# Kernel optimization log

Hardware: AMD Instinct MI355X
Metric: run time of the kernel (lower is better)

The kernel has to match this reference:

```python
import jax, jax.numpy as jnp
import numpy as np

VOXEL = 0.1          # superpoint_voxel_size
NUM_BATCHES = 4      # B (batch indices in coords[:,0] are in [0, B))


def setup_inputs() -> dict:
    key = jax.random.key(0)
    k1, k2, k3, k4, k5, k6, k7 = jax.random.split(key, 7)
    N, D = 1_000_000, 64
    batch_ids = jax.random.randint(k1, (N,), 0, NUM_BATCHES).astype(jnp.float32)
    xyz = jax.random.uniform(k2, (N, 3), dtype=jnp.float32) * 50.0  # 50m scene
    coords = jnp.concatenate([batch_ids[:, None], xyz], axis=1)      # (N,4)
    features = jax.random.normal(k3, (N, D), dtype=jnp.float32)
    s1 = 1.0 / np.sqrt(3.0)
    s2 = 1.0 / np.sqrt(D)
    W1 = jax.random.uniform(k4, (3, D), minval=-s1, maxval=s1, dtype=jnp.float32)
    b1 = jax.random.uniform(k5, (D,), minval=-s1, maxval=s1, dtype=jnp.float32)
    W2 = jax.random.uniform(k6, (D, D), minval=-s2, maxval=s2, dtype=jnp.float32)
    b2 = jax.random.uniform(k7, (D,), minval=-s2, maxval=s2, dtype=jnp.float32)
    return {"coords": coords, "features": features, "W1": W1, "b1": b1, "W2": W2, "b2": b2}


def reference(coords, features, W1, b1, W2, b2):
    N, D = features.shape
    batch_ids = coords[:, 0].astype(jnp.int32)          # (N,)
    xyz = coords[:, 1:4]                                 # (N,3)
    q = jnp.floor(xyz / VOXEL).astype(jnp.int32)         # voxel quantization
    combined = jnp.concatenate([batch_ids[:, None], q], axis=1)  # (N,4) int32 keys

    # torch.unique(dim=0, return_inverse=True): lexicographically sorted unique
    # rows. We pad to a fixed S=N segments (fill rows sorted to the tail via a
    # max sentinel); `valid` masks out the padding.
    SENT = jnp.iinfo(jnp.int32).max
    unique_sp, sp_to_point = jnp.unique(
        combined, axis=0, size=N, fill_value=SENT, return_inverse=True)
    sp_to_point = sp_to_point.reshape(-1)                # (N,)

    counts = jax.ops.segment_sum(jnp.ones((N,), jnp.float32), sp_to_point, num_segments=N)
    valid = counts > 0
    c = jnp.maximum(counts, 1.0)[:, None]                # clamp(min=1)

    sp_features = jax.ops.segment_sum(features, sp_to_point, num_segments=N) / c  # (N,D) mean
    sp_centers = jax.ops.segment_sum(xyz, sp_to_point, num_segments=N) / c        # (N,3) mean

    # pos_enc: Linear(3,D) -> ReLU -> Linear(D,D)
    pos = jnp.maximum(sp_centers @ W1 + b1, 0.0) @ W2 + b2
    sp_features = jnp.where(valid[:, None], sp_features + pos, 0.0)
    sp_centers = jnp.where(valid[:, None], sp_centers, 0.0)

    # batch_offsets: cumulative superpoint counts per batch (padding -> dump bin B)
    sp_batch = jnp.where(valid, unique_sp[:, 0], NUM_BATCHES)
    per_batch = jax.ops.segment_sum(jnp.ones((N,), jnp.int32), sp_batch,
                                    num_segments=NUM_BATCHES + 1)[:NUM_BATCHES]
    batch_offsets = jnp.concatenate([jnp.zeros((1,), jnp.int32), jnp.cumsum(per_batch)])
    return sp_features, sp_centers, sp_to_point, batch_offsets
```

## Files before the change

### kernel.cpp

```cpp
#include <hip/hip_runtime.h>
#include <stdint.h>


static constexpr uint32_t NWORDS = 1u << 24;
static constexpr uint32_t NBLK   = NWORDS / 1024;
static constexpr uint32_t MCAP   = 65536;

typedef __attribute__((ext_vector_type(8))) short short8;
typedef __attribute__((ext_vector_type(4))) float f32x4;

__device__ __forceinline__ short f2bf(float x) {
    union { float f; uint32_t u; } v; v.f = x;
    uint32_t u = v.u;
    uint32_t r = (u + 0x7FFFu + ((u >> 16) & 1u)) >> 16;
    return (short)r;
}

__device__ __forceinline__ uint32_t point_key(float4 c) {
    uint32_t b  = (uint32_t)(int)c.x;
    uint32_t qx = (uint32_t)(int)floorf(c.y / 0.1f);
    uint32_t qy = (uint32_t)(int)floorf(c.z / 0.1f);
    uint32_t qz = (uint32_t)(int)floorf(c.w / 0.1f);
    return (b << 27) | (qx << 18) | (qy << 9) | qz;
}

__global__ void k0_w2t(const float* __restrict__ W2, short* __restrict__ W2T) {
    int t = blockIdx.x * 256 + threadIdx.x;
    if (t < 4096) {
        int col = t >> 6, k = t & 63;
        W2T[col * 64 + k] = f2bf(W2[k * 64 + col]);
    }
}

__global__ void k1_keys(const float4* __restrict__ coords, uint32_t* __restrict__ bitmap, int N) {
    int i = blockIdx.x * blockDim.x + threadIdx.x;
    if (i >= N) return;
    uint32_t key = point_key(coords[i]);
    atomicOr(&bitmap[key >> 5], 1u << (key & 31u));
}

__global__ __launch_bounds__(256) void k2a_blockscan(
        const uint4* __restrict__ bm4, uint16_t* __restrict__ scan4,
        uint32_t* __restrict__ bsum) {
    int t = threadIdx.x;
    int lane = t & 63, wid = t >> 6;
    uint4 v = bm4[(size_t)blockIdx.x * 256 + t];
    uint32_t pc = __popc(v.x) + __popc(v.y) + __popc(v.z) + __popc(v.w);
    uint32_t sc = pc;
    #pragma unroll
    for (int off = 1; off < 64; off <<= 1) {
        uint32_t n = __shfl_up(sc, off);
        if (lane >= off) sc += n;
    }
    __shared__ uint32_t wt[4];
    if (lane == 63) wt[wid] = sc;
    __syncthreads();
    uint32_t wbase = 0;
    #pragma unroll
    for (int w = 0; w < 4; ++w) wbase += (w < wid) ? wt[w] : 0u;
    scan4[(size_t)blockIdx.x * 256 + t] = (uint16_t)(wbase + sc - pc);
    if (t == 255) bsum[blockIdx.x] = wbase + sc;
}

__global__ void k2b_topscan(const uint32_t* __restrict__ bsum, uint32_t* __restrict__ bscan) {
    __shared__ uint32_t s[1024];
    int t = threadIdx.x;
    uint32_t base = (uint32_t)t * 16u;
    const uint4* b4 = (const uint4*)(bsum + base);
    uint32_t sum = 0;
    #pragma unroll
    for (int k = 0; k < 4; ++k) { uint4 v = b4[k]; sum += v.x + v.y + v.z + v.w; }
    s[t] = sum;
    __syncthreads();
    for (int off = 1; off < 1024; off <<= 1) {
        uint32_t v = (t >= off) ? s[t - off] : 0u;
        __syncthreads();
        s[t] += v;
        __syncthreads();
    }
    uint32_t run = s[t] - sum;
    for (int k = 0; k < 16; ++k) { bscan[base + k] = run; run += bsum[base + k]; }
    if (t == 1023) bscan[16384] = run;
}

__global__ void k3a_rank(const float4* __restrict__ coords,
                         uint32_t* __restrict__ ranks,
                         const uint32_t* __restrict__ bitmap,
                         const uint16_t* __restrict__ scan4,
                         const uint32_t* __restrict__ bscan,
                         float* __restrict__ sums,
                         uint32_t* __restrict__ inv,
                         uint32_t* __restrict__ slotmap,
                         uint32_t* __restrict__ mctr,
                         float* __restrict__ msum,
                         float* __restrict__ mfeat,
                         float* __restrict__ out_sp, int N) {
    int i = blockIdx.x * blockDim.x + threadIdx.x;
    if (i >= N) return;
    float4 c = coords[i];
    uint32_t key = point_key(c);
    uint32_t w = key >> 5, bit = key & 31u;
    uint4 q = *(const uint4*)(bitmap + (w & ~3u));
    uint32_t wd[4] = {q.x, q.y, q.z, q.w};
    uint32_t idx = w & 3u;
    uint32_t r = bscan[w >> 10] + (uint32_t)scan4[w >> 2];
    uint32_t cur = 0;
    #pragma unroll
    for (uint32_t j = 0; j < 4; ++j) {
        r += (j < idx) ? __popc(wd[j]) : 0u;
        cur = (j == idx) ? wd[j] : cur;
    }
    r += __popc(cur & ((1u << bit) - 1u));
    ranks[i] = r;
    inv[r] = (uint32_t)i;
    out_sp[i] = (float)r;
    float* s4 = sums + 4u * (size_t)r;
    float old = atomicAdd(s4 + 0, 1.0f);
    s4[1] = c.y; s4[2] = c.z; s4[3] = c.w;
    if (old == 1.0f) {
        uint32_t slot = atomicAdd(mctr, 1u);
        if (slot < MCAP) {
            slotmap[r] = slot + 1u;
            float4 z = make_float4(0.f, 0.f, 0.f, 0.f);
            *(float4*)(msum + 4u * (size_t)slot) = z;
            float4* fz = (float4*)(mfeat + 64u * (size_t)slot);
            #pragma unroll
            for (int qq = 0; qq < 16; ++qq) fz[qq] = z;
        }
    }
}

__global__ void k3fix(const float4* __restrict__ coords,
                      const float* __restrict__ features,
                      const uint32_t* __restrict__ ranks,
                      const uint32_t* __restrict__ slotmap,
                      const float4* __restrict__ sums,
                      float* __restrict__ msum,
                      float* __restrict__ mfeat, int N) {
    int i = blockIdx.x * blockDim.x + threadIdx.x;
    if (i >= N) return;
    uint32_t r = ranks[i];
    uint32_t sl = slotmap[r];
    if (sl == 0) return;
    sl -= 1u;
    float cnt = sums[r].x;
    float4 c = coords[i];
    float* m = msum + 4u * (size_t)sl;
    atomicAdd(m + 0, c.y);
    atomicAdd(m + 1, c.z);
    atomicAdd(m + 2, c.w);
    float iv = 1.0f / cnt;
    const float* frow = features + (size_t)i * 64;
    float* orow = mfeat + (size_t)sl * 64;
    #pragma unroll 1
    for (int qq = 0; qq < 64; ++qq) atomicAdd(&orow[qq], frow[qq] * iv);
}

__global__ __launch_bounds__(256) void k5_fused(
        const f32x4* __restrict__ features4,
        const uint32_t* __restrict__ inv,
        const float4* __restrict__ sums,
        const uint32_t* __restrict__ slotmap,
        const float4* __restrict__ msum,
        const f32x4* __restrict__ mfeat4,
        const float* __restrict__ W1, const float* __restrict__ b1,
        const short* __restrict__ W2T, const float* __restrict__ b2,
        f32x4* __restrict__ out_feat4, float* __restrict__ out_cent, int N) {
    int lane = threadIdx.x & 63;
    int rows_base = blockIdx.x * 256 + (threadIdx.x >> 6) * 64;

    float4 sg4[4]; float cntg[4]; uint32_t invg[4];
    #pragma unroll
    for (int g = 0; g < 4; ++g) {
        int rg = rows_base + (g << 4) + (lane & 15);
        int rgc = rg < N ? rg : N - 1;
        sg4[g] = sums[rgc];
        cntg[g] = sg4[g].x;
        invg[g] = inv[rgc];
    }

    float scx[4], scy[4], scz[4];
    #pragma unroll
    for (int g = 0; g < 4; ++g) {
        int rg = rows_base + (g << 4) + (lane & 15);
        int rgc = rg < N ? rg : N - 1;
        float sx = sg4[g].y, sy = sg4[g].z, sz = sg4[g].w;
        if (cntg[g] > 1.5f) {
            float4 m = msum[slotmap[rgc] - 1u];
            sx = m.x; sy = m.y; sz = m.z;
        }
        float ic = cntg[g] > 0.f ? 1.f / cntg[g] : 0.f;
        scx[g] = sx * ic; scy[g] = sy * ic; scz[g] = sz * ic;
    }

    int my = rows_base + lane;
    if (my < N) {
        float4 s4 = sums[my];
        float sx = s4.y, sy = s4.z, sz = s4.w;
        if (s4.x > 1.5f) {
            float4 m = msum[slotmap[my] - 1u];
            sx = m.x; sy = m.y; sz = m.z;
        }
        float ic = s4.x > 0.f ? 1.f / s4.x : 0.f;
        out_cent[3 * (size_t)my + 0] = sx * ic;
        out_cent[3 * (size_t)my + 1] = sy * ic;
        out_cent[3 * (size_t)my + 2] = sz * ic;
    }

    f32x4 acc[4][4];
    #pragma unroll
    for (int cg = 0; cg < 4; ++cg) {
        f32x4 bv = ((const f32x4*)b2)[(cg << 2) + (lane >> 4)];
        #pragma unroll
        for (int g = 0; g < 4; ++g)
            acc[g][cg] = bv;
    }

    #pragma unroll
    for (int s = 0; s < 2; ++s) {
        int kb = s * 32 + ((lane >> 4) << 3);
        float4 tx0 = *(const float4*)(W1 + kb),       tx1 = *(const float4*)(W1 + kb + 4);
        float4 ty0 = *(const float4*)(W1 + 64 + kb),  ty1 = *(const float4*)(W1 + 64 + kb + 4);
        float4 tz0 = *(const float4*)(W1 + 128 + kb), tz1 = *(const float4*)(W1 + 128 + kb + 4);
        float4 tb0 = *(const float4*)(b1 + kb),       tb1 = *(const float4*)(b1 + kb + 4);
        float w1x[8] = {tx0.x, tx0.y, tx0.z, tx0.w, tx1.x, tx1.y, tx1.z, tx1.w};
        float w1y[8] = {ty0.x, ty0.y, ty0.z, ty0.w, ty1.x, ty1.y, ty1.z, ty1.w};
        float w1z[8] = {tz0.x, tz0.y, tz0.z, tz0.w, tz1.x, tz1.y, tz1.z, tz1.w};
        float b1v[8] = {tb0.x, tb0.y, tb0.z, tb0.w, tb1.x, tb1.y, tb1.z, tb1.w};

        short8 afrag[4];
        #pragma unroll
        for (int cg = 0; cg < 4; ++cg) {
            int col = (cg << 4) | (lane & 15);
            afrag[cg] = *(const short8*)(W2T + col * 64 + kb);
        }

        #pragma unroll
        for (int g = 0; g < 4; ++g) {
            short8 hf;
            #pragma unroll
            for (int j = 0; j < 8; ++j) {
                float h = fmaf(scz[g], w1z[j], fmaf(scy[g], w1y[j], fmaf(scx[g], w1x[j], b1v[j])));
                hf[j] = f2bf(fmaxf(h, 0.0f));
            }
            #pragma unroll
            for (int cg = 0; cg < 4; ++cg)
                acc[g][cg] = __builtin_amdgcn_mfma_f32_16x16x32_bf16(afrag[cg], hf, acc[g][cg], 0, 0, 0);
        }
    }

    #pragma unroll
    for (int g = 0; g < 4; ++g) {
        int gr = rows_base + (g << 4) + (lane & 15);
        if (gr >= N) continue;
        float cnt = cntg[g];
        f32x4 v[4];
        #pragma unroll
        for (int cg = 0; cg < 4; ++cg) v[cg] = acc[g][cg];
        if (cnt == 0.0f) {
            #pragma unroll
            for (int cg = 0; cg < 4; ++cg) v[cg] = (f32x4){0.f, 0.f, 0.f, 0.f};
        } else if (cnt == 1.0f) {
            size_t fb = (size_t)invg[g] * 16 + (lane >> 4);
            #pragma unroll
            for (int cg = 0; cg < 4; ++cg) v[cg] += features4[fb + (cg << 2)];
        } else {
            size_t mb = (size_t)(slotmap[gr] - 1u) * 16 + (lane >> 4);
            #pragma unroll
            for (int cg = 0; cg < 4; ++cg) v[cg] += mfeat4[mb + (cg << 2)];
        }
        size_t ob = (size_t)gr * 16 + (lane >> 4);
        #pragma unroll
        for (int cg = 0; cg < 4; ++cg)
            __builtin_nontemporal_store(v[cg], out_feat4 + ob + (cg << 2));
    }
}

__global__ void k6_offsets(const uint32_t* __restrict__ bscan, float* __restrict__ out_off) {
    int t = threadIdx.x;
    if (t < 5) {
        uint32_t v;
        if (t == 0)      v = 0u;
        else if (t == 4) v = bscan[16384];
        else             v = bscan[(uint32_t)t << 12];
        out_off[t] = (float)v;
    }
}

extern "C" void kernel_launch(void* const* d_in, const int* in_sizes, int n_in,
                              void* d_out, int out_size, void* d_ws, size_t ws_size,
                              hipStream_t stream) {
    const float4* coords = (const float4*)d_in[0];
    const float*  feats  = (const float*)d_in[1];
    const float*  W1 = (const float*)d_in[2];
    const float*  b1 = (const float*)d_in[3];
    const float*  W2 = (const float*)d_in[4];
    const float*  b2 = (const float*)d_in[5];
    int N = in_sizes[0] / 4;

    char* ws = (char*)d_ws;
    size_t o = 0;
    uint32_t* bitmap = (uint32_t*)(ws + o); o += (size_t)NWORDS * 4;
    uint16_t* scan4  = (uint16_t*)(ws + o); o += (size_t)(NWORDS / 4) * 2;
    uint32_t* bsum   = (uint32_t*)(ws + o); o += (size_t)NBLK * 4;
    uint32_t* bscan  = (uint32_t*)(ws + o); o += (size_t)(NBLK + 1) * 4;
    o = (o + 15) & ~(size_t)15;
    uint32_t* ranks  = (uint32_t*)(ws + o); o += (size_t)N * 4;
    o = (o + 15) & ~(size_t)15;
    float*    sums   = (float*)(ws + o);    o += (size_t)N * 16;
    uint32_t* inv    = (uint32_t*)(ws + o); o += (size_t)N * 4;
    o = (o + 15) & ~(size_t)15;
    short*    W2T    = (short*)(ws + o);    o += 8192;
    size_t multi_base = o;
    uint32_t* slotmap = (uint32_t*)(ws + o); o += (size_t)N * 4;
    uint32_t* mctr    = (uint32_t*)(ws + o); o += 16;
    size_t multi_size = o - multi_base;
    float*    msum    = (float*)(ws + o);    o += (size_t)MCAP * 16;
    float*    mfeat   = (float*)(ws + o);    o += (size_t)MCAP * 256;

    float* out_feat = (float*)d_out;
    float* out_cent = out_feat + (size_t)N * 64;
    float* out_sp   = out_cent + (size_t)N * 3;
    float* out_off  = out_sp + N;

    hipMemsetAsync(bitmap, 0, (size_t)NWORDS * 4, stream);
    hipMemsetAsync(sums, 0, (size_t)N * 16, stream);
    hipMemsetAsync(ws + multi_base, 0, multi_size, stream);

    int nb = (N + 255) / 256;
    k0_w2t<<<16, 256, 0, stream>>>(W2, W2T);
    k1_keys<<<nb, 256, 0, stream>>>(coords, bitmap, N);
    k2a_blockscan<<<NBLK, 256, 0, stream>>>((const uint4*)bitmap, scan4, bsum);
    k2b_topscan<<<1, 1024, 0, stream>>>(bsum, bscan);
    k3a_rank<<<nb, 256, 0, stream>>>(coords, ranks, bitmap, scan4, bscan, sums, inv,
                                     slotmap, mctr, msum, mfeat, out_sp, N);
    k3fix<<<nb, 256, 0, stream>>>(coords, feats, ranks, slotmap, (const float4*)sums,
                                  msum, mfeat, N);
    k5_fused<<<nb, 256, 0, stream>>>((const f32x4*)feats, inv, (const float4*)sums,
                                     slotmap, (const float4*)msum, (const f32x4*)mfeat,
                                     W1, b1, W2T, b2, (f32x4*)out_feat, out_cent, N);
    k6_offsets<<<1, 64, 0, stream>>>(bscan, out_off);
}
```

Measured before the change: 328.1 us.

## Pack per-segment count, slot, coords and inverse index into one 32-byte record

Merges the separate sums, inv and slotmap arrays into a single 32-byte-per-segment record holding count, slot id, coordinate sums and the source point index. This lets k3fix and k5_fused read one or two aligned float4 loads per segment instead of scattered loads from three arrays, and drops the separate slotmap memset. In exchange the zeroed workspace grows from 20 to 32 bytes per segment. The final output stores also switch from nontemporal to ordinary stores, which changes cache behaviour.

Measured after the change: 337.3 us. +2.8%, slower.

```diff
diff --git a/kernel.cpp b/kernel.cpp
--- a/kernel.cpp
+++ b/kernel.cpp
@@ -88,9 +88,7 @@
                          const uint32_t* __restrict__ bitmap,
                          const uint16_t* __restrict__ scan4,
                          const uint32_t* __restrict__ bscan,
-                         float* __restrict__ sums,
-                         uint32_t* __restrict__ inv,
-                         uint32_t* __restrict__ slotmap,
+                         float* __restrict__ psum,
                          uint32_t* __restrict__ mctr,
                          float* __restrict__ msum,
                          float* __restrict__ mfeat,
@@ -112,15 +110,14 @@
     }
     r += __popc(cur & ((1u << bit) - 1u));
     ranks[i] = r;
-    inv[r] = (uint32_t)i;
     out_sp[i] = (float)r;
-    float* s4 = sums + 4u * (size_t)r;
-    float old = atomicAdd(s4 + 0, 1.0f);
-    s4[1] = c.y; s4[2] = c.z; s4[3] = c.w;
+    float* p = psum + 8u * (size_t)r;
+    float old = atomicAdd(p, 1.0f);
+    *(float4*)(p + 4) = make_float4(c.y, c.z, c.w, __uint_as_float((uint32_t)i));
     if (old == 1.0f) {
         uint32_t slot = atomicAdd(mctr, 1u);
         if (slot < MCAP) {
-            slotmap[r] = slot + 1u;
+            *(uint32_t*)(p + 1) = slot + 1u;
             float4 z = make_float4(0.f, 0.f, 0.f, 0.f);
             *(float4*)(msum + 4u * (size_t)slot) = z;
             float4* fz = (float4*)(mfeat + 64u * (size_t)slot);
@@ -133,17 +130,17 @@
 __global__ void k3fix(const float4* __restrict__ coords,
                       const float* __restrict__ features,
                       const uint32_t* __restrict__ ranks,
-                      const uint32_t* __restrict__ slotmap,
-                      const float4* __restrict__ sums,
+                      const float4* __restrict__ psum4,
                       float* __restrict__ msum,
                       float* __restrict__ mfeat, int N) {
     int i = blockIdx.x * blockDim.x + threadIdx.x;
     if (i >= N) return;
     uint32_t r = ranks[i];
-    uint32_t sl = slotmap[r];
+    float4 q0 = psum4[2 * (size_t)r];
+    uint32_t sl = __float_as_uint(q0.y);
     if (sl == 0) return;
     sl -= 1u;
-    float cnt = sums[r].x;
+    float cnt = q0.x;
     float4 c = coords[i];
     float* m = msum + 4u * (size_t)sl;
     atomicAdd(m + 0, c.y);
@@ -158,9 +155,7 @@
 
 __global__ __launch_bounds__(256) void k5_fused(
         const f32x4* __restrict__ features4,
-        const uint32_t* __restrict__ inv,
-        const float4* __restrict__ sums,
-        const uint32_t* __restrict__ slotmap,
+        const float4* __restrict__ psum4,
         const float4* __restrict__ msum,
         const f32x4* __restrict__ mfeat4,
         const float* __restrict__ W1, const float* __restrict__ b1,
@@ -169,39 +164,38 @@
     int lane = threadIdx.x & 63;
     int rows_base = blockIdx.x * 256 + (threadIdx.x >> 6) * 64;
 
-    float4 sg4[4]; float cntg[4]; uint32_t invg[4];
+    float cntg[4], scx[4], scy[4], scz[4];
+    uint32_t invg[4], slotg[4];
     #pragma unroll
     for (int g = 0; g < 4; ++g) {
         int rg = rows_base + (g << 4) + (lane & 15);
         int rgc = rg < N ? rg : N - 1;
-        sg4[g] = sums[rgc];
-        cntg[g] = sg4[g].x;
-        invg[g] = inv[rgc];
-    }
-
-    float scx[4], scy[4], scz[4];
-    #pragma unroll
-    for (int g = 0; g < 4; ++g) {
-        int rg = rows_base + (g << 4) + (lane & 15);
-        int rgc = rg < N ? rg : N - 1;
-        float sx = sg4[g].y, sy = sg4[g].z, sz = sg4[g].w;
-        if (cntg[g] > 1.5f) {
-            float4 m = msum[slotmap[rgc] - 1u];
+        float4 q0 = psum4[2 * (size_t)rgc];
+        float4 q1 = psum4[2 * (size_t)rgc + 1];
+        float cnt = q0.x;
+        cntg[g] = cnt;
+        slotg[g] = __float_as_uint(q0.y);
+        invg[g] = __float_as_uint(q1.w);
+        float sx = q1.x, sy = q1.y, sz = q1.z;
+        if (cnt > 1.5f) {
+            float4 m = msum[slotg[g] - 1u];
             sx = m.x; sy = m.y; sz = m.z;
         }
-        float ic = cntg[g] > 0.f ? 1.f / cntg[g] : 0.f;
+        float ic = cnt > 0.f ? 1.f / cnt : 0.f;
         scx[g] = sx * ic; scy[g] = sy * ic; scz[g] = sz * ic;
     }
 
     int my = rows_base + lane;
     if (my < N) {
-        float4 s4 = sums[my];
-        float sx = s4.y, sy = s4.z, sz = s4.w;
-        if (s4.x > 1.5f) {
-            float4 m = msum[slotmap[my] - 1u];
+        float4 q0 = psum4[2 * (size_t)my];
+        float4 q1 = psum4[2 * (size_t)my + 1];
+        float cnt = q0.x;
+        float sx = q1.x, sy = q1.y, sz = q1.z;
+        if (cnt > 1.5f) {
+            float4 m = msum[__float_as_uint(q0.y) - 1u];
             sx = m.x; sy = m.y; sz = m.z;
         }
-        float ic = s4.x > 0.f ? 1.f / s4.x : 0.f;
+        float ic = cnt > 0.f ? 1.f / cnt : 0.f;
         out_cent[3 * (size_t)my + 0] = sx * ic;
         out_cent[3 * (size_t)my + 1] = sy * ic;
         out_cent[3 * (size_t)my + 2] = sz * ic;
@@ -265,14 +259,14 @@
             #pragma unroll
             for (int cg = 0; cg < 4; ++cg) v[cg] += features4[fb + (cg << 2)];
         } else {
-            size_t mb = (size_t)(slotmap[gr] - 1u) * 16 + (lane >> 4);
+            size_t mb = (size_t)(slotg[g] - 1u) * 16 + (lane >> 4);
             #pragma unroll
             for (int cg = 0; cg < 4; ++cg) v[cg] += mfeat4[mb + (cg << 2)];
         }
         size_t ob = (size_t)gr * 16 + (lane >> 4);
         #pragma unroll
         for (int cg = 0; cg < 4; ++cg)
-            __builtin_nontemporal_store(v[cg], out_feat4 + ob + (cg << 2));
+            out_feat4[ob + (cg << 2)] = v[cg];
     }
 }
 
@@ -304,19 +298,14 @@
     uint16_t* scan4  = (uint16_t*)(ws + o); o += (size_t)(NWORDS / 4) * 2;
     uint32_t* bsum   = (uint32_t*)(ws + o); o += (size_t)NBLK * 4;
     uint32_t* bscan  = (uint32_t*)(ws + o); o += (size_t)(NBLK + 1) * 4;
-    o = (o + 15) & ~(size_t)15;
+    o = (o + 31) & ~(size_t)31;
+    float*    psum   = (float*)(ws + o);    o += (size_t)N * 32;
     uint32_t* ranks  = (uint32_t*)(ws + o); o += (size_t)N * 4;
     o = (o + 15) & ~(size_t)15;
-    float*    sums   = (float*)(ws + o);    o += (size_t)N * 16;
-    uint32_t* inv    = (uint32_t*)(ws + o); o += (size_t)N * 4;
-    o = (o + 15) & ~(size_t)15;
     short*    W2T    = (short*)(ws + o);    o += 8192;
-    size_t multi_base = o;
-    uint32_t* slotmap = (uint32_t*)(ws + o); o += (size_t)N * 4;
-    uint32_t* mctr    = (uint32_t*)(ws + o); o += 16;
-    size_t multi_size = o - multi_base;
-    float*    msum    = (float*)(ws + o);    o += (size_t)MCAP * 16;
-    float*    mfeat   = (float*)(ws + o);    o += (size_t)MCAP * 256;
+    uint32_t* mctr   = (uint32_t*)(ws + o); o += 16;
+    float*    msum   = (float*)(ws + o);    o += (size_t)MCAP * 16;
+    float*    mfeat  = (float*)(ws + o);    o += (size_t)MCAP * 256;
 
     float* out_feat = (float*)d_out;
     float* out_cent = out_feat + (size_t)N * 64;
@@ -324,20 +313,19 @@
     float* out_off  = out_sp + N;
 
     hipMemsetAsync(bitmap, 0, (size_t)NWORDS * 4, stream);
-    hipMemsetAsync(sums, 0, (size_t)N * 16, stream);
-    hipMemsetAsync(ws + multi_base, 0, multi_size, stream);
+    hipMemsetAsync(psum, 0, (size_t)N * 32, stream);
+    hipMemsetAsync(mctr, 0, 16, stream);
 
     int nb = (N + 255) / 256;
     k0_w2t<<<16, 256, 0, stream>>>(W2, W2T);
     k1_keys<<<nb, 256, 0, stream>>>(coords, bitmap, N);
     k2a_blockscan<<<NBLK, 256, 0, stream>>>((const uint4*)bitmap, scan4, bsum);
     k2b_topscan<<<1, 1024, 0, stream>>>(bsum, bscan);
-    k3a_rank<<<nb, 256, 0, stream>>>(coords, ranks, bitmap, scan4, bscan, sums, inv,
-                                     slotmap, mctr, msum, mfeat, out_sp, N);
-    k3fix<<<nb, 256, 0, stream>>>(coords, feats, ranks, slotmap, (const float4*)sums,
-                                  msum, mfeat, N);
-    k5_fused<<<nb, 256, 0, stream>>>((const f32x4*)feats, inv, (const float4*)sums,
-                                     slotmap, (const float4*)msum, (const f32x4*)mfeat,
+    k3a_rank<<<nb, 256, 0, stream>>>(coords, ranks, bitmap, scan4, bscan, psum,
+                                     mctr, msum, mfeat, out_sp, N);
+    k3fix<<<nb, 256, 0, stream>>>(coords, feats, ranks, (const float4*)psum, msum, mfeat, N);
+    k5_fused<<<nb, 256, 0, stream>>>((const f32x4*)feats, (const float4*)psum,
+                                     (const float4*)msum, (const f32x4*)mfeat,
                                      W1, b1, W2T, b2, (f32x4*)out_feat, out_cent, N);
     k6_offsets<<<1, 64, 0, stream>>>(bscan, out_off);
 }
```
